# Kernel tuning notes

Hardware: AMD Instinct MI355X
Metric: run time of the kernel (lower is better)

The kernel has to match this reference:

```python
import jax, jax.numpy as jnp
import numpy as np
import math

# ---- static configuration (mirrors __init__ kwargs) ----
G, M = 64, 128              # graphs x atoms-per-graph
N = G * M                   # 8192 nodes
NUM_RADIAL = 16
DENSITY_W = 1.0
PROJ_W = np.linspace(0.5, 3.0, NUM_RADIAL)
# e^2/(4*pi*eps0) = 14.3996... eV*Angstrom; FIELD_CONSTANT/(4*pi) is used in the code
FIELD_CONSTANT = 4.0 * np.pi * 14.399645351950548
KC = FIELD_CONSTANT / (4.0 * np.pi)

def _dfact(n):
    return 1 if n <= 1 else n * _dfact(n - 2)

def _cl_sigma(l, s, norm):
    # GTO g_l(r) ~ r^l exp(-r^2/(2 s^2)).
    if norm == 'multipoles':   # unit multipole moment normalization
        return 1.0 / ((2.0 * np.pi) ** 1.5 * s ** (3 + 2 * l) * _dfact(2 * l + 1))
    # 'receiver': L2-normalized radial GTO
    return 1.0 / np.sqrt(np.pi ** 1.5 * s ** (3 + 2 * l) * _dfact(2 * l + 1) / 2.0 ** l)

# buffers (registered in __init__)
TOTAL_W = jnp.asarray(np.sqrt((DENSITY_W ** 2 + PROJ_W ** 2) / 2.0), jnp.float32)          # [S]
L0F = jnp.asarray([_cl_sigma(0, s, 'receiver') / _cl_sigma(0, s, 'multipoles') for s in PROJ_W], jnp.float32)
L1W = jnp.asarray([math.sqrt(3.0) * s * s * _cl_sigma(1, s, 'receiver') / _cl_sigma(0, s, 'multipoles') for s in PROJ_W], jnp.float32)
SQRT_PI = math.sqrt(math.pi)
DIP_IDX = np.array([3, 1, 2])   # source_feats columns -> cartesian dipole (x,y,z)


def setup_inputs() -> dict:
    key = jax.random.key(0)
    k1, k2 = jax.random.split(key)
    source_feats = jax.random.normal(k1, (N, 4), jnp.float32) * 0.5       # [q, mu_y, mu_z, mu_x]
    node_positions = jax.random.uniform(k2, (N, 3), jnp.float32) * 12.0   # Angstrom box
    batch = jnp.asarray(np.repeat(np.arange(G), M), jnp.int32)
    # per-graph complete directed graph without self loops (matches the torch helper with N=1)
    base = np.arange(M)
    row = np.repeat(base, M); col = np.tile(base, M)
    keep = row != col
    row, col = row[keep], col[keep]
    off = (np.arange(G) * M)[:, None]
    sender = (row[None, :] + off).reshape(-1)
    receiver = (col[None, :] + off).reshape(-1)
    edge_index = jnp.asarray(np.stack([sender, receiver]), jnp.int32)     # [2, E]
    return {"source_feats": source_feats, "node_positions": node_positions,
            "batch": batch, "edge_index": edge_index}


def _forward(source_feats, node_positions, edge_index):
    n_nodes = node_positions.shape[0]
    S = NUM_RADIAL
    sender, receiver = edge_index[0], edge_index[1]
    R = node_positions[receiver] - node_positions[sender]          # [E,3]
    r = jnp.linalg.norm(R, axis=-1)
    r_e = jnp.maximum(r, 1e-10)[:, None]                           # [E,1]
    Rhat = R / r_e                                                 # [E,3]
    w = TOTAL_W[None, :]                                           # [1,S]
    g_s = jnp.exp(-r_e ** 2 / (4.0 * w ** 2)) / (w * SQRT_PI)      # [E,S]
    T_s = jax.scipy.special.erf(r_e / (2.0 * w)) / r_e             # [E,S]
    fp_s = (g_s - T_s) / r_e                                       # [E,S]
    q_j = source_feats[sender, 0]                                  # [E]
    mu_j = source_feats[sender][:, DIP_IDX]                        # [E,3]
    mu_Rhat = jnp.sum(mu_j * Rhat, axis=-1)                        # [E]
    # l=0 channels
    contrib_l0 = q_j[:, None] * T_s - mu_Rhat[:, None] * fp_s      # [E,S]
    feat_l0 = jax.ops.segment_sum(contrib_l0, receiver, num_segments=n_nodes)
    feat_l0 = KC * L0F[None, :] * feat_l0                          # [N,S]
    # l=1 channels
    fp_over_r = fp_s / r_e
    fpp_s = -g_s / (2.0 * w ** 2) - 2.0 * g_s / r_e ** 2 + 2.0 * T_s / r_e ** 2
    contrib_l1 = fp_s[..., None] * Rhat[:, None, :] * q_j[:, None, None]              # [E,S,3]
    contrib_l1 = contrib_l1 - fp_over_r[..., None] * mu_j[:, None, :]
    contrib_l1 = contrib_l1 + ((fp_over_r - fpp_s) * mu_Rhat[:, None])[..., None] * Rhat[:, None, :]
    E = contrib_l1.shape[0]
    feat_l1 = jax.ops.segment_sum(contrib_l1.reshape(E, -1), receiver, num_segments=n_nodes)
    feat_l1 = KC * L1W[None, :, None] * feat_l1.reshape(n_nodes, S, 3)                # [N,S,3]
    # output layout: [l0 (S) | interleaved (y,z,x) per radial (3S)]
    out_l1 = feat_l1[:, :, np.array([1, 2, 0])].reshape(n_nodes, 3 * S)
    features = jnp.concatenate([feat_l0, out_l1], axis=1)                             # [N,4S]
    # GTO self-interaction (r -> 0 analytic limits): T(0)=1/(w sqrt(pi)), fp(0)=0,
    # fp_over_r(0) = -1/(6 w^3 sqrt(pi)), fp_over_r(0)-fpp(0) = 0.
    q = source_feats[:, 0]
    si_l0 = KC * L0F[None, :] * q[:, None] / (TOTAL_W[None, :] * SQRT_PI)             # [N,S]
    mu = source_feats[:, DIP_IDX]                                                     # [N,3]
    si_coef = KC * L1W / (6.0 * TOTAL_W ** 3 * SQRT_PI)                               # [S]
    si_l1 = si_coef[None, :, None] * mu[:, None, np.array([1, 2, 0])]                 # [N,S,3] in (y,z,x)
    si_terms = jnp.concatenate([si_l0, si_l1.reshape(n_nodes, 3 * S)], axis=1)        # [N,4S]
    return features, si_terms


def reference(source_feats, node_positions, batch, edge_index):
    # batch only determines edge_index (precomputed statically in setup_inputs)
    features, si_terms = _forward(source_feats, node_positions, edge_index)
    # include_self_interaction=False -> features returned unmodified; module returns (features, si_terms, None)
    return (features, si_terms)
```

## Files before the change

kernel.cpp:

```cpp
#include <hip/hip_runtime.h>

#define NNODES 8192
#define MNODES 128
#define NS 16
#define NP 8
#define RPB 16
#define CHUNKS 16
#define BLOCK (RPB*CHUNKS)

typedef float v2f __attribute__((ext_vector_type(2)));

constexpr double csqrt_(double x) {
  double g = x > 1.0 ? x : 1.0;
  for (int i = 0; i < 100; ++i) g = 0.5 * (g + x / g);
  return g;
}

struct CTab {
  float inv2w[NS], cexp[NS], c1[NS], i2w2[NS], sl0[NS], sl1[NS], si0[NS], si1[NS];
  constexpr CTab() : inv2w{}, cexp{}, c1{}, i2w2{}, sl0{}, sl1{}, si0{}, si1{} {
    const double PI = 3.14159265358979323846;
    const double KC = 14.399645351950548;
    const double SP = csqrt_(PI);
    const double p2pi15 = 2.0 * PI * csqrt_(2.0 * PI);
    const double pi15 = PI * csqrt_(PI);
    for (int s = 0; s < NS; ++s) {
      const double sig = 0.5 + s * (2.5 / 15.0);
      const double w = csqrt_((1.0 + sig * sig) * 0.5);
      const double s3 = sig * sig * sig;
      const double cl0m = 1.0 / (p2pi15 * s3);
      const double cl0r = 1.0 / csqrt_(pi15 * s3);
      const double cl1r = 1.0 / csqrt_(pi15 * s3 * sig * sig * 1.5);
      const double L0F = cl0r / cl0m;
      const double L1W = csqrt_(3.0) * sig * sig * cl1r / cl0m;
      inv2w[s] = (float)(0.5 / w);
      cexp[s]  = (float)(-1.4426950408889634 * 0.25 / (w * w));
      c1[s]    = (float)(1.0 / (w * SP));
      i2w2[s]  = (float)(0.5 / (w * w));
      sl0[s]   = (float)(KC * L0F);
      sl1[s]   = (float)(KC * L1W);
      si0[s]   = (float)(KC * L0F / (w * SP));
      si1[s]   = (float)(KC * L1W / (6.0 * w * w * w * SP));
    }
  }
};
constexpr CTab CT{};

__global__ __launch_bounds__(BLOCK, 2)
void elec_feat_kernel(const float* __restrict__ feats,
                      const float* __restrict__ pos,
                      float* __restrict__ out)
{
  __shared__ __align__(16) float4 spq[MNODES];
  __shared__ __align__(16) float4 smu[MNODES];
  __shared__ __align__(16) float sfeat[RPB * 64];
  __shared__ __align__(16) float ssi[RPB * 64];

  const int tid = threadIdx.x;
  const int g = blockIdx.x >> 3;
  const int rbase = (blockIdx.x & 7) * RPB;
  const int nodebase = g * MNODES;

  if (tid < MNODES) {
    const int n = nodebase + tid;
    const float4 f = reinterpret_cast<const float4*>(feats)[n];
    spq[tid] = make_float4(pos[3 * n], pos[3 * n + 1], pos[3 * n + 2], f.x);
    smu[tid] = make_float4(f.w, f.y, f.z, 0.f);
  }
  __syncthreads();

  const int chunk = tid & (CHUNKS - 1);
  const int rsub = tid >> 4;
  const int rl = rbase + rsub;

  const float4 rp = spq[rl];

  v2f A0[NP], AX[NP], AY[NP], AZ[NP];
#pragma unroll
  for (int p = 0; p < NP; ++p) {
    A0[p] = (v2f){0.f, 0.f}; AX[p] = (v2f){0.f, 0.f};
    AY[p] = (v2f){0.f, 0.f}; AZ[p] = (v2f){0.f, 0.f};
  }

  for (int k = 0; k < MNODES / CHUNKS; ++k) {
    const int j = (k << 4) | chunk;
    const float4 sp = spq[j];
    const float4 sm = smu[j];
    const bool self = (j == rl);
    const float Rx = rp.x - sp.x, Ry = rp.y - sp.y, Rz = rp.z - sp.z;
    float r2 = fmaf(Rx, Rx, fmaf(Ry, Ry, Rz * Rz));
    r2 = fmaxf(r2, 1e-12f);
    const float inv_r = __builtin_amdgcn_rsqf(r2);
    const float r = r2 * inv_r;
    const float hx = Rx * inv_r, hy = Ry * inv_r, hz = Rz * inv_r;
    const float qj = self ? 0.f : sp.w;
    const float m0 = self ? 0.f : sm.x;
    const float m1 = self ? 0.f : sm.y;
    const float m2 = self ? 0.f : sm.z;
    const float muR = fmaf(m0, hx, fmaf(m1, hy, m2 * hz));

#pragma unroll
    for (int p = 0; p < NP; ++p) {
      const v2f cI = {CT.inv2w[2 * p], CT.inv2w[2 * p + 1]};
      const v2f cE = {CT.cexp[2 * p],  CT.cexp[2 * p + 1]};
      const v2f cC = {CT.c1[2 * p],    CT.c1[2 * p + 1]};
      const v2f cW = {CT.i2w2[2 * p],  CT.i2w2[2 * p + 1]};
      const v2f ea = cE * r2;
      v2f e;
      e.x = __builtin_amdgcn_exp2f(ea.x);
      e.y = __builtin_amdgcn_exp2f(ea.y);
      const v2f x = cI * r;
      const v2f ta = 0.47047f * x + 1.0f;
      v2f t;
      t.x = __builtin_amdgcn_rcpf(ta.x);
      t.y = __builtin_amdgcn_rcpf(ta.y);
      v2f pp = 0.7478556f * t - 0.0958798f;
      pp = pp * t + 0.3480242f;
      pp = pp * t;
      const v2f erfv = 1.0f - pp * e;
      const v2f T = erfv * inv_r;
      const v2f gs = cC * e;
      const v2f fp = (gs - T) * inv_r;
      const v2f fpr = fp * inv_r;
      const v2f t2 = 3.0f * fpr + gs * cW;
      A0[p] += qj * T - muR * fp;
      const v2f ca = muR * t2 + fp * qj;
      AX[p] += ca * hx - fpr * m0;
      AY[p] += ca * hy - fpr * m1;
      AZ[p] += ca * hz - fpr * m2;
    }
  }

#pragma unroll
  for (int p = 0; p < NP; ++p) {
#pragma unroll
    for (int m = 1; m < CHUNKS; m <<= 1) {
      A0[p].x += __shfl_xor(A0[p].x, m); A0[p].y += __shfl_xor(A0[p].y, m);
      AX[p].x += __shfl_xor(AX[p].x, m); AX[p].y += __shfl_xor(AX[p].y, m);
      AY[p].x += __shfl_xor(AY[p].x, m); AY[p].y += __shfl_xor(AY[p].y, m);
      AZ[p].x += __shfl_xor(AZ[p].x, m); AZ[p].y += __shfl_xor(AZ[p].y, m);
    }
  }

  if (chunk == 0) {
    float* F = &sfeat[rsub * 64];
    float* Si = &ssi[rsub * 64];
#pragma unroll
    for (int s = 0; s < NS; ++s) {
      const int p = s >> 1, c = s & 1;
      const float a0 = c ? A0[p].y : A0[p].x;
      const float axv = c ? AX[p].y : AX[p].x;
      const float ayv = c ? AY[p].y : AY[p].x;
      const float azv = c ? AZ[p].y : AZ[p].x;
      F[s] = CT.sl0[s] * a0;
      F[16 + 3 * s + 0] = CT.sl1[s] * ayv;
      F[16 + 3 * s + 1] = CT.sl1[s] * azv;
      F[16 + 3 * s + 2] = CT.sl1[s] * axv;
    }
    const float qr = spq[rl].w;
    const float4 mr = smu[rl];
#pragma unroll
    for (int s = 0; s < NS; ++s) {
      Si[s] = CT.si0[s] * qr;
      Si[16 + 3 * s + 0] = CT.si1[s] * mr.y;
      Si[16 + 3 * s + 1] = CT.si1[s] * mr.z;
      Si[16 + 3 * s + 2] = CT.si1[s] * mr.x;
    }
  }
  __syncthreads();

  const size_t i0 = (size_t)(nodebase + rbase);
  float4* df = reinterpret_cast<float4*>(out + i0 * 64);
  float4* ds = reinterpret_cast<float4*>(out + (size_t)NNODES * 64 + i0 * 64);
  df[tid] = reinterpret_cast<const float4*>(sfeat)[tid];
  ds[tid] = reinterpret_cast<const float4*>(ssi)[tid];
}

extern "C" void kernel_launch(void* const* d_in, const int* in_sizes, int n_in,
                              void* d_out, int out_size, void* d_ws, size_t ws_size,
                              hipStream_t stream) {
  const float* feats = (const float*)d_in[0];
  const float* pos = (const float*)d_in[1];
  float* out = (float*)d_out;
  hipLaunchKernelGGL(elec_feat_kernel, dim3(NNODES / RPB), dim3(BLOCK), 0, stream,
                     feats, pos, out);
}
```

Before: 79.10 us.

## Split radial channels across thread halves to halve per-thread accumulator state

Each receiver row is now handled by two 16-lane groups, each computing half of the 16 radial channels, with 8 rows per block and blocks twice as numerous. This halves the per-thread accumulator registers and is meant to raise occupancy (launch bounds now allow 4 blocks per CU). The per-channel constants are hoisted into registers. The pair geometry (distance, rsqrt, direction, muR) is now computed twice per pair, once in each half, and the node data is staged into shared memory twice as often because there are more blocks.

```diff
diff --git a/kernel.cpp b/kernel.cpp
--- a/kernel.cpp
+++ b/kernel.cpp
@@ -3,10 +3,11 @@
 #define NNODES 8192
 #define MNODES 128
 #define NS 16
-#define NP 8
-#define RPB 16
+#define SPLIT 2
+#define NP (NS / (2 * SPLIT))
+#define RPB 8
 #define CHUNKS 16
-#define BLOCK (RPB*CHUNKS)
+#define BLOCK (RPB * CHUNKS * SPLIT)
 
 typedef float v2f __attribute__((ext_vector_type(2)));
 
@@ -46,7 +47,7 @@
 };
 constexpr CTab CT{};
 
-__global__ __launch_bounds__(BLOCK, 2)
+__global__ __launch_bounds__(BLOCK, 4)
 void elec_feat_kernel(const float* __restrict__ feats,
                       const float* __restrict__ pos,
                       float* __restrict__ out)
@@ -57,8 +58,8 @@
   __shared__ __align__(16) float ssi[RPB * 64];
 
   const int tid = threadIdx.x;
-  const int g = blockIdx.x >> 3;
-  const int rbase = (blockIdx.x & 7) * RPB;
+  const int g = blockIdx.x >> 4;
+  const int rbase = (blockIdx.x & 15) * RPB;
   const int nodebase = g * MNODES;
 
   if (tid < MNODES) {
@@ -70,8 +71,20 @@
   __syncthreads();
 
   const int chunk = tid & (CHUNKS - 1);
-  const int rsub = tid >> 4;
+  const int shalf = (tid >> 4) & (SPLIT - 1);
+  const int rsub = tid >> 5;
   const int rl = rbase + rsub;
+  const int sb = shalf * (2 * NP);
+
+  v2f cI[NP], cE[NP], cC[NP], cW[NP];
+#pragma unroll
+  for (int p = 0; p < NP; ++p) {
+    const int s0 = sb + 2 * p;
+    cI[p] = (v2f){CT.inv2w[s0], CT.inv2w[s0 + 1]};
+    cE[p] = (v2f){CT.cexp[s0],  CT.cexp[s0 + 1]};
+    cC[p] = (v2f){CT.c1[s0],    CT.c1[s0 + 1]};
+    cW[p] = (v2f){CT.i2w2[s0],  CT.i2w2[s0 + 1]};
+  }
 
   const float4 rp = spq[rl];
 
@@ -101,15 +114,11 @@
 
 #pragma unroll
     for (int p = 0; p < NP; ++p) {
-      const v2f cI = {CT.inv2w[2 * p], CT.inv2w[2 * p + 1]};
-      const v2f cE = {CT.cexp[2 * p],  CT.cexp[2 * p + 1]};
-      const v2f cC = {CT.c1[2 * p],    CT.c1[2 * p + 1]};
-      const v2f cW = {CT.i2w2[2 * p],  CT.i2w2[2 * p + 1]};
-      const v2f ea = cE * r2;
+      const v2f ea = cE[p] * r2;
       v2f e;
       e.x = __builtin_amdgcn_exp2f(ea.x);
       e.y = __builtin_amdgcn_exp2f(ea.y);
-      const v2f x = cI * r;
+      const v2f x = cI[p] * r;
       const v2f ta = 0.47047f * x + 1.0f;
       v2f t;
       t.x = __builtin_amdgcn_rcpf(ta.x);
@@ -119,10 +128,10 @@
       pp = pp * t;
       const v2f erfv = 1.0f - pp * e;
       const v2f T = erfv * inv_r;
-      const v2f gs = cC * e;
+      const v2f gs = cC[p] * e;
       const v2f fp = (gs - T) * inv_r;
       const v2f fpr = fp * inv_r;
-      const v2f t2 = 3.0f * fpr + gs * cW;
+      const v2f t2 = 3.0f * fpr + gs * cW[p];
       A0[p] += qj * T - muR * fp;
       const v2f ca = muR * t2 + fp * qj;
       AX[p] += ca * hx - fpr * m0;
@@ -146,8 +155,9 @@
     float* F = &sfeat[rsub * 64];
     float* Si = &ssi[rsub * 64];
 #pragma unroll
-    for (int s = 0; s < NS; ++s) {
-      const int p = s >> 1, c = s & 1;
+    for (int i = 0; i < 2 * NP; ++i) {
+      const int s = sb + i;
+      const int p = i >> 1, c = i & 1;
       const float a0 = c ? A0[p].y : A0[p].x;
       const float axv = c ? AX[p].y : AX[p].x;
       const float ayv = c ? AY[p].y : AY[p].x;
@@ -160,7 +170,8 @@
     const float qr = spq[rl].w;
     const float4 mr = smu[rl];
 #pragma unroll
-    for (int s = 0; s < NS; ++s) {
+    for (int i = 0; i < 2 * NP; ++i) {
+      const int s = sb + i;
       Si[s] = CT.si0[s] * qr;
       Si[16 + 3 * s + 0] = CT.si1[s] * mr.y;
       Si[16 + 3 * s + 1] = CT.si1[s] * mr.z;
@@ -170,10 +181,13 @@
   __syncthreads();
 
   const size_t i0 = (size_t)(nodebase + rbase);
-  float4* df = reinterpret_cast<float4*>(out + i0 * 64);
-  float4* ds = reinterpret_cast<float4*>(out + (size_t)NNODES * 64 + i0 * 64);
-  df[tid] = reinterpret_cast<const float4*>(sfeat)[tid];
-  ds[tid] = reinterpret_cast<const float4*>(ssi)[tid];
+  if (tid < RPB * 16) {
+    float4* df = reinterpret_cast<float4*>(out + i0 * 64);
+    df[tid] = reinterpret_cast<const float4*>(sfeat)[tid];
+  } else {
+    float4* dsi = reinterpret_cast<float4*>(out + (size_t)NNODES * 64 + i0 * 64);
+    dsi[tid - RPB * 16] = reinterpret_cast<const float4*>(ssi)[tid - RPB * 16];
+  }
 }
 
 extern "C" void kernel_launch(void* const* d_in, const int* in_sizes, int n_in,
```

Result: faster. 76.31 us (-3.5%).
